# Performance work log

Hardware: AMD Instinct MI355X
Metric: run time of the kernel (lower is better)

Reference implementation:

```python
import jax, jax.numpy as jnp
import numpy as np

N0, N1, N2 = 100000, 25000, 6250
E0, E1, E2 = 600000, 150000, 37500
K = 6


def cheb_conv(x, edge_index, W, b):
    """torch_geometric ChebConv with sym normalization, lambda_max=2:
    L_hat = -D^{-1/2} A D^{-1/2}; T0=x, T1=L_hat x, Tk=2 L_hat T_{k-1} - T_{k-2}."""
    n = x.shape[0]
    src, dst = edge_index[0], edge_index[1]
    deg = jax.ops.segment_sum(jnp.ones(src.shape[0], x.dtype), src, num_segments=n)
    dinv = jnp.where(deg > 0, jax.lax.rsqrt(jnp.maximum(deg, 1.0)), 0.0)
    w = -(dinv[src] * dinv[dst])  # [E]

    def prop(h):  # (L_hat h)_i = sum_{j->i} w_ij h_j
        return jax.ops.segment_sum(w[:, None] * h[src], dst, num_segments=n)

    Tx0 = x
    out = Tx0 @ W[0]
    Tx1 = prop(x)
    out = out + Tx1 @ W[1]
    for k in range(2, W.shape[0]):
        Tx2 = 2.0 * prop(Tx1) - Tx0
        out = out + Tx2 @ W[k]
        Tx0, Tx1 = Tx1, Tx2
    return out + b


def pool(x, rows, cols, vals, n_out):
    # sparse.mm(D, x): y[r] += v * x[c]
    return jax.ops.segment_sum(vals[:, None] * x[cols], rows, num_segments=n_out)


def setup_inputs() -> dict:
    key = jax.random.key(0)
    ks = jax.random.split(key, 16)
    inp = {}
    inp["x"] = jax.random.normal(ks[0], (N0, 3), jnp.float32)
    inp["edge_index0"] = jax.random.randint(ks[1], (2, E0), 0, N0, jnp.int32)
    inp["edge_index1"] = jax.random.randint(ks[2], (2, E1), 0, N1, jnp.int32)
    inp["edge_index2"] = jax.random.randint(ks[3], (2, E2), 0, N2, jnp.int32)
    s = 0.05
    inp["W0"] = jax.random.normal(ks[4], (K, 3, 128), jnp.float32) * s
    inp["b0"] = jax.random.normal(ks[5], (128,), jnp.float32) * s
    inp["W1"] = jax.random.normal(ks[6], (K, 128, 128), jnp.float32) * s
    inp["b1"] = jax.random.normal(ks[7], (128,), jnp.float32) * s
    inp["W2"] = jax.random.normal(ks[8], (K, 128, 256), jnp.float32) * s
    inp["b2"] = jax.random.normal(ks[9], (256,), jnp.float32) * s
    inp["D0_rows"] = jax.random.randint(ks[10], (100000,), 0, N1, jnp.int32)
    inp["D0_cols"] = jax.random.randint(ks[11], (100000,), 0, N0, jnp.int32)
    inp["D0_vals"] = jax.random.uniform(ks[12], (100000,), jnp.float32)
    inp["D1_rows"] = jax.random.randint(ks[13], (25000,), 0, N2, jnp.int32)
    inp["D1_cols"] = jax.random.randint(ks[14], (25000,), 0, N1, jnp.int32)
    inp["D1_vals"] = jax.random.uniform(ks[15], (25000,), jnp.float32)
    k2 = jax.random.split(jax.random.fold_in(key, 1), 2)
    inp["linW"] = jax.random.normal(k2[0], (10, N2 * 256), jnp.float32) * 0.001
    inp["linb"] = jax.random.normal(k2[1], (10,), jnp.float32) * s
    return inp


def reference(x, edge_index0, edge_index1, edge_index2, W0, b0, W1, b1, W2, b2,
              D0_rows, D0_cols, D0_vals, D1_rows, D1_cols, D1_vals, linW, linb):
    h = jax.nn.relu(cheb_conv(x, edge_index0, W0, b0))      # [N0,128]
    h = pool(h, D0_rows, D0_cols, D0_vals, N1)               # [N1,128]
    h = jax.nn.relu(cheb_conv(h, edge_index1, W1, b1))      # [N1,128]
    h = pool(h, D1_rows, D1_cols, D1_vals, N2)               # [N2,128]
    h = cheb_conv(h, edge_index2, W2, b2)                    # [N2,256]
    Z = linW @ h.reshape(-1) + linb                           # [10]
    return Z
```

## Files before the change

kernel.cpp:

```cpp
#include <hip/hip_runtime.h>


namespace {
constexpr int cN0 = 100000, cN1 = 25000, cN2 = 6250;
constexpr int cE0 = 600000, cE1 = 150000, cE2 = 37500;
constexpr int cD  = cN2 * 256;

constexpr int JN[5]  = {cN0, cN1, cN2, cN1, cN2};
constexpr int JE[5]  = {cE0, cE1, cE2, 100000, 25000};
constexpr int JB[5]  = {391, 98, 25, 98, 25};
constexpr int JBBASE[6] = {0, 391, 489, 514, 612, 637};
constexpr int TB = 637;
constexpr int JCB[5] = {293, 74, 19, 49, 13};
constexpr int JCBASE[6] = {0, 293, 367, 386, 435, 448};
constexpr int TCB = 448;
constexpr int CHUNK = 2048;
constexpr int BSTRIDE = 400;

constexpr int EBASE[5]   = {0, 600000, 750000, 787500, 887500};
constexpr int E_TOTAL    = 912500;
constexpr int NBASE[5]   = {0, 100096, 125184, 131584, 156672};
constexpr int NPAD_TOTAL = 163072;
constexpr int DEGBASE[3] = {0, 100000, 125000};
constexpr int DEG_TOTAL  = 131250;
constexpr int WPREP_TOTAL = 768 * 128 + 768 * 256 + 128 * 32;
}

typedef __attribute__((ext_vector_type(8))) short short8;
typedef __attribute__((ext_vector_type(4))) float floatx4;

__device__ inline ushort f2bf(float f) {
  union { float f; unsigned u; } v; v.f = f;
  unsigned u = v.u;
  return (ushort)((u + 0x7FFFu + ((u >> 16) & 1u)) >> 16);
}

__device__ inline float bf2f(unsigned lo16) {
  return __uint_as_float(lo16 << 16);
}

__device__ inline int job_of_cb(int cb) {
  int j = 0;
  while (cb >= JCBASE[j + 1]) ++j;
  return j;
}
__device__ inline int job_of_bucket(int g) {
  int j = 0;
  while (g >= JBBASE[j + 1]) ++j;
  return j;
}

__global__ __launch_bounds__(256) void c1_count_kernel(
    const int* __restrict__ k0, const int* __restrict__ k1, const int* __restrict__ k2,
    const int* __restrict__ k3, const int* __restrict__ k4,
    const int* __restrict__ s0, const int* __restrict__ s1, const int* __restrict__ s2,
    int* __restrict__ degcnt, int* __restrict__ cntCB) {
  __shared__ int cnt[BSTRIDE];
  int cb = blockIdx.x;
  int j = job_of_cb(cb);
  int lb = cb - JCBASE[j];
  const int* keys;
  const int* srck = nullptr;
  int dbase = 0;
  switch (j) {
    case 0: keys = k0; srck = s0; dbase = DEGBASE[0]; break;
    case 1: keys = k1; srck = s1; dbase = DEGBASE[1]; break;
    case 2: keys = k2; srck = s2; dbase = DEGBASE[2]; break;
    case 3: keys = k3; break;
    default: keys = k4; break;
  }
  int nB = JB[j];
  for (int b = threadIdx.x; b < nB; b += 256) cnt[b] = 0;
  __syncthreads();
  int e0 = lb * CHUNK;
  int e1 = min(e0 + CHUNK, JE[j]);
  for (int e = e0 + threadIdx.x; e < e1; e += 256) {
    atomicAdd(&cnt[keys[e] >> 8], 1);
    if (srck) atomicAdd(&degcnt[dbase + srck[e]], 1);
  }
  __syncthreads();
  for (int b = threadIdx.x; b < nB; b += 256)
    cntCB[cb * BSTRIDE + b] = cnt[b];
}

__global__ __launch_bounds__(256) void c2a_scan_kernel(int* __restrict__ cntCB,
                                                       int* __restrict__ bucketTot,
                                                       const int* __restrict__ degcnt,
                                                       float* __restrict__ dinv) {
  __shared__ int s[256];
  int g = blockIdx.x;
  int j = job_of_bucket(g);
  int b = g - JBBASE[j];
  int cb0 = JCBASE[j], nCB = JCB[j];
  int carry = 0;
  for (int c0 = 0; c0 < nCB; c0 += 256) {
    int i = c0 + threadIdx.x;
    int v = (i < nCB) ? cntCB[(cb0 + i) * BSTRIDE + b] : 0;
    s[threadIdx.x] = v;
    __syncthreads();
    for (int d = 1; d < 256; d <<= 1) {
      int t = (threadIdx.x >= d) ? s[threadIdx.x - d] : 0;
      __syncthreads();
      s[threadIdx.x] += t;
      __syncthreads();
    }
    if (i < nCB) cntCB[(cb0 + i) * BSTRIDE + b] = carry + s[threadIdx.x] - v;
    carry += s[255];
    __syncthreads();
  }
  if (threadIdx.x == 0) bucketTot[g] = carry;
  int idx = blockIdx.x * 256 + threadIdx.x;
  if (idx < DEG_TOTAL) {
    int c = degcnt[idx];
    dinv[idx] = (c > 0) ? rsqrtf((float)c) : 0.f;
  }
}

__global__ __launch_bounds__(256) void c2b_scan_kernel(const int* __restrict__ bucketTot,
                                                       int* __restrict__ bucketBase) {
  __shared__ int s[256];
  int j = blockIdx.x;
  int g0 = JBBASE[j], nB = JB[j];
  int carry = 0;
  for (int c0 = 0; c0 < nB; c0 += 256) {
    int i = c0 + threadIdx.x;
    int v = (i < nB) ? bucketTot[g0 + i] : 0;
    s[threadIdx.x] = v;
    __syncthreads();
    for (int d = 1; d < 256; d <<= 1) {
      int t = (threadIdx.x >= d) ? s[threadIdx.x - d] : 0;
      __syncthreads();
      s[threadIdx.x] += t;
      __syncthreads();
    }
    if (i < nB) bucketBase[g0 + i] = carry + s[threadIdx.x] - v;
    carry += s[255];
    __syncthreads();
  }
}

__global__ __launch_bounds__(256) void c3_dst_kernel(
    const int* __restrict__ d0, const int* __restrict__ s0,
    const int* __restrict__ d1, const int* __restrict__ s1,
    const int* __restrict__ d2, const int* __restrict__ s2,
    const int* __restrict__ p0r, const int* __restrict__ p0c, const float* __restrict__ p0v,
    const int* __restrict__ p1r, const int* __restrict__ p1c, const float* __restrict__ p1v,
    const float* __restrict__ dinv,
    const int* __restrict__ cntCB, const int* __restrict__ bucketBase,
    int2* __restrict__ scatPairs) {
  __shared__ int base[BSTRIDE];
  int cb = blockIdx.x;
  int j = job_of_cb(cb);
  int lb = cb - JCBASE[j];
  const int* dk; const int* sk; const float* vv = nullptr;
  switch (j) {
    case 0: dk = d0; sk = s0; break;
    case 1: dk = d1; sk = s1; break;
    case 2: dk = d2; sk = s2; break;
    case 3: dk = p0r; sk = p0c; vv = p0v; break;
    default: dk = p1r; sk = p1c; vv = p1v; break;
  }
  int nB = JB[j];
  for (int b = threadIdx.x; b < nB; b += 256)
    base[b] = EBASE[j] + bucketBase[JBBASE[j] + b] + cntCB[cb * BSTRIDE + b];
  __syncthreads();
  int e0 = lb * CHUNK;
  int e1 = min(e0 + CHUNK, JE[j]);
  for (int e = e0 + threadIdx.x; e < e1; e += 256) {
    int d = dk[e];
    int s = sk[e];
    float w;
    if (j < 3) w = -(dinv[DEGBASE[j] + s] * dinv[DEGBASE[j] + d]);
    else w = vv[e];
    int pos = atomicAdd(&base[d >> 8], 1);
    scatPairs[pos] = make_int2(((d & 255) << 17) | s, __float_as_int(w));
  }
}

__global__ __launch_bounds__(256) void dcsr_kernel(const int2* __restrict__ scatPairs,
                                                   const int* __restrict__ bucketTot,
                                                   const int* __restrict__ bucketBase,
                                                   int* __restrict__ off,
                                                   int2* __restrict__ csrPairs) {
  __shared__ int cnt[256];
  __shared__ int sArr[256];
  __shared__ int cur[256];
  int g = blockIdx.x;
  int j = job_of_bucket(g);
  int b = g - JBBASE[j];
  int relBase = bucketBase[g];
  int st = EBASE[j] + relBase;
  int en = st + bucketTot[g];
  cnt[threadIdx.x] = 0;
  __syncthreads();
  for (int idx = st + threadIdx.x; idx < en; idx += 256)
    atomicAdd(&cnt[scatPairs[idx].x >> 17], 1);
  __syncthreads();
  int v = cnt[threadIdx.x];
  sArr[threadIdx.x] = v;
  __syncthreads();
  for (int d = 1; d < 256; d <<= 1) {
    int t = (threadIdx.x >= d) ? sArr[threadIdx.x - d] : 0;
    __syncthreads();
    sArr[threadIdx.x] += t;
    __syncthreads();
  }
  int excl = sArr[threadIdx.x] - v;
  int node = b * 256 + threadIdx.x;
  if (node < JN[j]) off[NBASE[j] + node] = relBase + excl;
  if (threadIdx.x == 0 && b == JB[j] - 1) off[NBASE[j] + JN[j]] = JE[j];
  cur[threadIdx.x] = st + excl;
  __syncthreads();
  for (int idx = st + threadIdx.x; idx < en; idx += 256) {
    int2 p = scatPairs[idx];
    int dl = p.x >> 17;
    int s = p.x & 0x1FFFF;
    int pos = atomicAdd(&cur[dl], 1);
    csrPairs[pos] = make_int2(s, p.y);
  }
}

__global__ __launch_bounds__(256) void csr_prop128_kernel(
    const int* __restrict__ off, const int2* __restrict__ pairs,
    const float* __restrict__ h, float* __restrict__ y, ushort* __restrict__ ybf,
    const float* __restrict__ prev, float scale, int N) {
  int r = blockIdx.x * 8 + (threadIdx.x >> 5);
  int l = threadIdx.x & 31;
  if (r >= N) return;
  int s = off[r], e = off[r + 1];
  const float4* h4 = (const float4*)h;
  float ax = 0.f, ay = 0.f, az = 0.f, aw = 0.f;
  int j = s;
  for (; j + 4 <= e; j += 4) {
    int2 p0 = pairs[j], p1 = pairs[j + 1], p2 = pairs[j + 2], p3 = pairs[j + 3];
    float4 v0 = h4[(size_t)p0.x * 32 + l];
    float4 v1 = h4[(size_t)p1.x * 32 + l];
    float4 v2 = h4[(size_t)p2.x * 32 + l];
    float4 v3 = h4[(size_t)p3.x * 32 + l];
    float w0 = __int_as_float(p0.y), w1 = __int_as_float(p1.y);
    float w2 = __int_as_float(p2.y), w3 = __int_as_float(p3.y);
    ax += w0 * v0.x + w1 * v1.x + w2 * v2.x + w3 * v3.x;
    ay += w0 * v0.y + w1 * v1.y + w2 * v2.y + w3 * v3.y;
    az += w0 * v0.z + w1 * v1.z + w2 * v2.z + w3 * v3.z;
    aw += w0 * v0.w + w1 * v1.w + w2 * v2.w + w3 * v3.w;
  }
  for (; j < e; ++j) {
    int2 p = pairs[j];
    float4 v0 = h4[(size_t)p.x * 32 + l];
    float w = __int_as_float(p.y);
    ax += w * v0.x; ay += w * v0.y; az += w * v0.z; aw += w * v0.w;
  }
  float4 v = make_float4(scale * ax, scale * ay, scale * az, scale * aw);
  if (prev) {
    float4 pv = ((const float4*)prev)[(size_t)r * 32 + l];
    v.x -= pv.x; v.y -= pv.y; v.z -= pv.z; v.w -= pv.w;
  }
  if (y) ((float4*)y)[(size_t)r * 32 + l] = v;
  uint2 sp = make_uint2(f2bf(v.x) | ((unsigned)f2bf(v.y) << 16),
                        f2bf(v.z) | ((unsigned)f2bf(v.w) << 16));
  ((uint2*)ybf)[(size_t)r * 32 + l] = sp;
}

__global__ __launch_bounds__(256) void csr_pool_bf16_kernel(
    const int* __restrict__ off, const int2* __restrict__ pairs,
    const ushort* __restrict__ hbf, float* __restrict__ y, ushort* __restrict__ ybf,
    int N) {
  int r = blockIdx.x * 8 + (threadIdx.x >> 5);
  int l = threadIdx.x & 31;
  if (r >= N) return;
  int s = off[r], e = off[r + 1];
  const uint2* h2 = (const uint2*)hbf;
  float ax = 0.f, ay = 0.f, az = 0.f, aw = 0.f;
  int j = s;
  for (; j + 4 <= e; j += 4) {
    int2 p0 = pairs[j], p1 = pairs[j + 1], p2 = pairs[j + 2], p3 = pairs[j + 3];
    uint2 v0 = h2[(size_t)p0.x * 32 + l];
    uint2 v1 = h2[(size_t)p1.x * 32 + l];
    uint2 v2 = h2[(size_t)p2.x * 32 + l];
    uint2 v3 = h2[(size_t)p3.x * 32 + l];
    float w0 = __int_as_float(p0.y), w1 = __int_as_float(p1.y);
    float w2 = __int_as_float(p2.y), w3 = __int_as_float(p3.y);
    ax += w0 * bf2f(v0.x & 0xFFFFu) + w1 * bf2f(v1.x & 0xFFFFu)
        + w2 * bf2f(v2.x & 0xFFFFu) + w3 * bf2f(v3.x & 0xFFFFu);
    ay += w0 * bf2f(v0.x >> 16) + w1 * bf2f(v1.x >> 16)
        + w2 * bf2f(v2.x >> 16) + w3 * bf2f(v3.x >> 16);
    az += w0 * bf2f(v0.y & 0xFFFFu) + w1 * bf2f(v1.y & 0xFFFFu)
        + w2 * bf2f(v2.y & 0xFFFFu) + w3 * bf2f(v3.y & 0xFFFFu);
    aw += w0 * bf2f(v0.y >> 16) + w1 * bf2f(v1.y >> 16)
        + w2 * bf2f(v2.y >> 16) + w3 * bf2f(v3.y >> 16);
  }
  for (; j < e; ++j) {
    int2 p = pairs[j];
    uint2 v0 = h2[(size_t)p.x * 32 + l];
    float w = __int_as_float(p.y);
    ax += w * bf2f(v0.x & 0xFFFFu);
    ay += w * bf2f(v0.x >> 16);
    az += w * bf2f(v0.y & 0xFFFFu);
    aw += w * bf2f(v0.y >> 16);
  }
  float4 v = make_float4(ax, ay, az, aw);
  ((float4*)y)[(size_t)r * 32 + l] = v;
  uint2 sp = make_uint2(f2bf(v.x) | ((unsigned)f2bf(v.y) << 16),
                        f2bf(v.z) | ((unsigned)f2bf(v.w) << 16));
  ((uint2*)ybf)[(size_t)r * 32 + l] = sp;
}

__global__ void csr_prop3_kernel(const int* __restrict__ off, const int2* __restrict__ pairs,
                                 const float4* __restrict__ h, float4* __restrict__ y,
                                 const float4* __restrict__ prev, float scale, int N,
                                 ushort* __restrict__ ybf, int kout) {
  int r = blockIdx.x * blockDim.x + threadIdx.x;
  if (r >= N) return;
  int s = off[r], e = off[r + 1];
  float ax = 0.f, ay = 0.f, az = 0.f;
  int j = s;
  for (; j + 4 <= e; j += 4) {
    int2 p0 = pairs[j], p1 = pairs[j + 1], p2 = pairs[j + 2], p3 = pairs[j + 3];
    float4 h0 = h[p0.x], h1 = h[p1.x], h2 = h[p2.x], h3 = h[p3.x];
    float w0 = __int_as_float(p0.y), w1 = __int_as_float(p1.y);
    float w2 = __int_as_float(p2.y), w3 = __int_as_float(p3.y);
    ax += w0 * h0.x + w1 * h1.x + w2 * h2.x + w3 * h3.x;
    ay += w0 * h0.y + w1 * h1.y + w2 * h2.y + w3 * h3.y;
    az += w0 * h0.z + w1 * h1.z + w2 * h2.z + w3 * h3.z;
  }
  for (; j < e; ++j) {
    int2 p = pairs[j];
    float4 hv = h[p.x];
    float w = __int_as_float(p.y);
    ax += w * hv.x; ay += w * hv.y; az += w * hv.z;
  }
  float4 v = make_float4(scale * ax, scale * ay, scale * az, 0.f);
  if (prev) {
    float4 pv = prev[r];
    v.x -= pv.x; v.y -= pv.y; v.z -= pv.z;
  }
  y[r] = v;
  uint2 sp = make_uint2(f2bf(v.x) | ((unsigned)f2bf(v.y) << 16), (unsigned)f2bf(v.z));
  *(uint2*)(ybf + (size_t)r * 32 + kout * 4) = sp;
}

__global__ void copyx_kernel(const float* __restrict__ x, float4* __restrict__ Tb,
                             ushort* __restrict__ Abf, int N) {
  int r = blockIdx.x * 256 + threadIdx.x;
  if (r >= N) return;
  float x0 = x[3 * r], x1 = x[3 * r + 1], x2 = x[3 * r + 2];
  Tb[r] = make_float4(x0, x1, x2, 0.f);
  uint4 z = make_uint4(0, 0, 0, 0);
  uint4 first = make_uint4(f2bf(x0) | ((unsigned)f2bf(x1) << 16), (unsigned)f2bf(x2), 0, 0);
  uint4* p = (uint4*)(Abf + (size_t)r * 32);
  p[0] = first; p[1] = z; p[2] = z; p[3] = z;
}

__global__ __launch_bounds__(256, 2) void h0_mfma_kernel(
    const ushort* __restrict__ Abf, const ushort* __restrict__ W0b,
    const float* __restrict__ b0, ushort* __restrict__ h0bf, int M) {
  __shared__ ushort Al[64][40];
  __shared__ ushort Bl[128][40];
  __shared__ ushort Hs[64][128];
  const int tid = threadIdx.x;
  const int rowBase = blockIdx.x * 64;
  const int wave = tid >> 6;
  const int lane = tid & 63;
  const int m16 = lane & 15;
  const int quad = lane >> 4;
  {
    int sRow = tid >> 2;
    int sK8 = (tid & 3) * 8;
    int row = rowBase + sRow;
    uint4 av = make_uint4(0, 0, 0, 0);
    if (row < M) av = *(const uint4*)(Abf + (size_t)row * 32 + sK8);
    *(uint4*)&Al[sRow][sK8] = av;
  }
#pragma unroll
  for (int l = 0; l < 2; ++l) {
    int lin = tid + l * 256;
    int bRow = lin >> 2;
    int bK8 = (lin & 3) * 8;
    *(uint4*)&Bl[bRow][bK8] = *(const uint4*)(W0b + (size_t)bRow * 32 + bK8);
  }
  __syncthreads();
  short8 a = *(const short8*)&Al[wave * 16 + m16][quad * 8];
  floatx4 acc[8];
#pragma unroll
  for (int c = 0; c < 8; ++c) {
    floatx4 z;
    z[0] = 0.f; z[1] = 0.f; z[2] = 0.f; z[3] = 0.f;
    short8 b = *(const short8*)&Bl[c * 16 + m16][quad * 8];
    acc[c] = __builtin_amdgcn_mfma_f32_16x16x32_bf16(a, b, z, 0, 0, 0);
  }
#pragma unroll
  for (int c = 0; c < 8; ++c) {
    int col = c * 16 + m16;
    float bv = b0[col];
#pragma unroll
    for (int r = 0; r < 4; ++r)
      Hs[wave * 16 + quad * 4 + r][col] = f2bf(fmaxf(acc[c][r] + bv, 0.f));
  }
  __syncthreads();
  const uint4* ls = (const uint4*)&Hs[0][0];
  uint4* gd = (uint4*)(h0bf + (size_t)rowBase * 128);
#pragma unroll
  for (int i = 0; i < 4; ++i) {
    int idx = tid + i * 256;
    if (rowBase + (idx >> 4) < M) gd[idx] = ls[idx];
  }
}

__global__ void prep_w_kernel(const float* __restrict__ W0, const float* __restrict__ W1,
                              const float* __restrict__ W2, ushort* __restrict__ W0b,
                              ushort* __restrict__ Wt1, ushort* __restrict__ Wt2,
                              int* __restrict__ degcnt) {
  int i = blockIdx.x * 256 + threadIdx.x;
  if (i < 768 * 128) {
    int k = i / 128, n = i - k * 128;
    Wt1[(size_t)n * 768 + k] = f2bf(W1[i]);
  } else if (i < 768 * 128 + 768 * 256) {
    int i2 = i - 768 * 128;
    int k = i2 / 256, n = i2 - k * 256;
    Wt2[(size_t)n * 768 + k] = f2bf(W2[i2]);
  } else if (i < WPREP_TOTAL) {
    int i3 = i - 768 * 128 - 768 * 256;
    int col = i3 >> 5, k = i3 & 31;
    int a = k >> 2, jj = k & 3;
    float v = (k < 24 && jj < 3) ? W0[(a * 3 + jj) * 128 + col] : 0.f;
    W0b[(size_t)col * 32 + k] = f2bf(v);
  } else {
    int i4 = i - WPREP_TOTAL;
    if (i4 < DEG_TOTAL) degcnt[i4] = 0;
  }
}

template <int RELU, int OUTBF>
__global__ __launch_bounds__(256, 2) void gemm_mfma_kernel(
    const ushort* __restrict__ Tbf, const ushort* __restrict__ Wt,
    const float* __restrict__ bias, float* __restrict__ C, ushort* __restrict__ Cb,
    int M, int N) {
  __shared__ ushort Al[64][40];
  __shared__ ushort Bl[128][40];
  __shared__ ushort Hs[64][128];
  const int tid = threadIdx.x;
  const int rowBase = blockIdx.x * 64;
  const int colBase = blockIdx.y * 128;
  const int wave = tid >> 6;
  const int lane = tid & 63;
  const int m16 = lane & 15;
  const int quad = lane >> 4;
  const size_t Mstride = (size_t)M * 128;

  floatx4 acc[8];
#pragma unroll
  for (int c = 0; c < 8; ++c)
#pragma unroll
    for (int r = 0; r < 4; ++r) acc[c][r] = 0.f;

  const int sRow = tid >> 2;
  const int sK8 = (tid & 3) * 8;
  const int growA = rowBase + sRow;
  const bool aValid = growA < M;

  for (int kc = 0; kc < 24; ++kc) {
    uint4 av = make_uint4(0, 0, 0, 0);
    if (aValid)
      av = *(const uint4*)(Tbf + (size_t)(kc >> 2) * Mstride + (size_t)growA * 128
                           + ((kc & 3) << 5) + sK8);
    *(uint4*)&Al[sRow][sK8] = av;
#pragma unroll
    for (int l = 0; l < 2; ++l) {
      int lin = tid + l * 256;
      int bRow = lin >> 2;
      int bK8 = (lin & 3) * 8;
      *(uint4*)&Bl[bRow][bK8] =
          *(const uint4*)(Wt + (size_t)(colBase + bRow) * 768 + kc * 32 + bK8);
    }
    __syncthreads();

    short8 a = *(const short8*)&Al[wave * 16 + m16][quad * 8];
#pragma unroll
    for (int c = 0; c < 8; ++c) {
      short8 b = *(const short8*)&Bl[c * 16 + m16][quad * 8];
      acc[c] = __builtin_amdgcn_mfma_f32_16x16x32_bf16(a, b, acc[c], 0, 0, 0);
    }
    __syncthreads();
  }

  if (OUTBF) {
#pragma unroll
    for (int c = 0; c < 8; ++c) {
      int col = c * 16 + m16;
      float bv = bias[col];
#pragma unroll
      for (int r = 0; r < 4; ++r) {
        float v = acc[c][r] + bv;
        if (RELU) v = fmaxf(v, 0.f);
        Hs[wave * 16 + quad * 4 + r][col] = f2bf(v);
      }
    }
    __syncthreads();
    const uint4* ls = (const uint4*)&Hs[0][0];
    uint4* gd = (uint4*)(Cb + (size_t)rowBase * 128);
#pragma unroll
    for (int i = 0; i < 4; ++i) {
      int idx = tid + i * 256;
      if (rowBase + (idx >> 4) < M) gd[idx] = ls[idx];
    }
  } else {
#pragma unroll
    for (int c = 0; c < 8; ++c) {
      int col = colBase + c * 16 + m16;
      float bv = bias[col];
#pragma unroll
      for (int r = 0; r < 4; ++r) {
        int row = rowBase + wave * 16 + quad * 4 + r;
        if (row < M) {
          float v = acc[c][r] + bv;
          if (RELU) v = fmaxf(v, 0.f);
          C[(size_t)row * N + col] = v;
        }
      }
    }
  }
}

__global__ void initout_kernel(float* __restrict__ out, const float* __restrict__ linb) {
  int i = threadIdx.x;
  if (i < 10) out[i] = linb[i];
}

__global__ __launch_bounds__(256) void linear_kernel(const float* __restrict__ Wl,
                                                     const float* __restrict__ h,
                                                     float* __restrict__ out, int D) {
  float p[10];
#pragma unroll
  for (int j = 0; j < 10; ++j) p[j] = 0.f;
  int stride = gridDim.x * blockDim.x;
  for (int i = blockIdx.x * blockDim.x + threadIdx.x; i < D; i += stride) {
    float hv = h[i];
#pragma unroll
    for (int j = 0; j < 10; ++j) p[j] += Wl[(size_t)j * D + i] * hv;
  }
#pragma unroll
  for (int j = 0; j < 10; ++j) {
#pragma unroll
    for (int off = 32; off > 0; off >>= 1) p[j] += __shfl_down(p[j], off, 64);
  }
  __shared__ float s[4][10];
  int wave = threadIdx.x >> 6, lane = threadIdx.x & 63;
  if (lane == 0) {
#pragma unroll
    for (int j = 0; j < 10; ++j) s[wave][j] = p[j];
  }
  __syncthreads();
  if (threadIdx.x < 10) {
    float t = s[0][threadIdx.x] + s[1][threadIdx.x] + s[2][threadIdx.x] + s[3][threadIdx.x];
    atomicAdd(&out[threadIdx.x], t);
  }
}

extern "C" void kernel_launch(void* const* d_in, const int* in_sizes, int n_in,
                              void* d_out, int out_size, void* d_ws, size_t ws_size,
                              hipStream_t stream) {
  const float* x    = (const float*)d_in[0];
  const int*   ei0  = (const int*)d_in[1];
  const int*   ei1  = (const int*)d_in[2];
  const int*   ei2  = (const int*)d_in[3];
  const float* W0   = (const float*)d_in[4];
  const float* b0   = (const float*)d_in[5];
  const float* W1   = (const float*)d_in[6];
  const float* b1   = (const float*)d_in[7];
  const float* W2   = (const float*)d_in[8];
  const float* b2   = (const float*)d_in[9];
  const int*   D0r  = (const int*)d_in[10];
  const int*   D0c  = (const int*)d_in[11];
  const float* D0v  = (const float*)d_in[12];
  const int*   D1r  = (const int*)d_in[13];
  const int*   D1c  = (const int*)d_in[14];
  const float* D1v  = (const float*)d_in[15];
  const float* linW = (const float*)d_in[16];
  const float* linb = (const float*)d_in[17];
  float* out = (float*)d_out;
  (void)in_sizes; (void)n_in; (void)out_size; (void)ws_size;

  const int* src0 = ei0;            const int* dst0 = ei0 + cE0;
  const int* src1 = ei1;            const int* dst1 = ei1 + cE1;
  const int* src2 = ei2;            const int* dst2 = ei2 + cE2;

  float* ws = (float*)d_ws;
  size_t off = 0;
  auto alloc = [&](size_t n) {
    float* p = ws + off;
    off += (n + 63) & ~size_t(63);
    return p;
  };
  float* dinv       = alloc(DEG_TOTAL);
  int*   degcnt     = (int*)alloc(DEG_TOTAL);
  int*   cntCB      = (int*)alloc((size_t)TCB * BSTRIDE);
  int*   bucketTot  = (int*)alloc(TB);
  int*   bucketBase = (int*)alloc(TB);
  int2*  scatPairs  = (int2*)alloc((size_t)2 * E_TOTAL);
  int2*  csrPairs   = (int2*)alloc((size_t)2 * E_TOTAL);
  int*   offArr     = (int*)alloc(NPAD_TOTAL);
  ushort* W0b       = (ushort*)alloc(128 * 32 / 2);
  ushort* Wt1       = (ushort*)alloc(768 * 128 / 2);
  ushort* Wt2       = (ushort*)alloc(768 * 256 / 2);
  float4* Tb0       = (float4*)alloc((size_t)6 * cN0 * 4);
  ushort* Abf0      = (ushort*)alloc((size_t)cN0 * 16);
  ushort* h0bf      = (ushort*)alloc((size_t)cN0 * 64);
  float* Tlvl1      = alloc((size_t)6 * cN1 * 128);
  ushort* Tbf1      = (ushort*)alloc((size_t)6 * cN1 * 64);
  ushort* out1b     = (ushort*)alloc((size_t)cN1 * 64);
  float* Tlvl2      = alloc((size_t)6 * cN2 * 128);
  ushort* Tbf2      = (ushort*)alloc((size_t)6 * cN2 * 64);
  float* out2       = alloc((size_t)cN2 * 256);

  auto nb = [](long long n) { return (unsigned)((n + 255) / 256); };

  prep_w_kernel<<<nb(WPREP_TOTAL + DEG_TOTAL), 256, 0, stream>>>(
      W0, W1, W2, W0b, Wt1, Wt2, degcnt);

  c1_count_kernel<<<TCB, 256, 0, stream>>>(dst0, dst1, dst2, D0r, D1r,
                                           src0, src1, src2, degcnt, cntCB);
  c2a_scan_kernel<<<TB, 256, 0, stream>>>(cntCB, bucketTot, degcnt, dinv);
  c2b_scan_kernel<<<5, 256, 0, stream>>>(bucketTot, bucketBase);
  c3_dst_kernel<<<TCB, 256, 0, stream>>>(dst0, src0, dst1, src1, dst2, src2,
                                         D0r, D0c, D0v, D1r, D1c, D1v,
                                         dinv, cntCB, bucketBase, scatPairs);
  dcsr_kernel<<<TB, 256, 0, stream>>>(scatPairs, bucketTot, bucketBase,
                                      offArr, csrPairs);

  auto seg_off   = [&](int s) { return offArr + NBASE[s]; };
  auto seg_pairs = [&](int s) { return csrPairs + EBASE[s]; };

  copyx_kernel<<<nb(cN0), 256, 0, stream>>>(x, Tb0, Abf0, cN0);
  {
    auto Tk = [&](int k) { return Tb0 + (size_t)k * cN0; };
    csr_prop3_kernel<<<nb(cN0), 256, 0, stream>>>(seg_off(0), seg_pairs(0),
        Tk(0), Tk(1), nullptr, 1.f, cN0, Abf0, 1);
    csr_prop3_kernel<<<nb(cN0), 256, 0, stream>>>(seg_off(0), seg_pairs(0),
        Tk(1), Tk(2), Tk(0), 2.f, cN0, Abf0, 2);
    csr_prop3_kernel<<<nb(cN0), 256, 0, stream>>>(seg_off(0), seg_pairs(0),
        Tk(2), Tk(3), Tk(1), 2.f, cN0, Abf0, 3);
    csr_prop3_kernel<<<nb(cN0), 256, 0, stream>>>(seg_off(0), seg_pairs(0),
        Tk(3), Tk(4), Tk(2), 2.f, cN0, Abf0, 4);
    csr_prop3_kernel<<<nb(cN0), 256, 0, stream>>>(seg_off(0), seg_pairs(0),
        Tk(4), Tk(5), Tk(3), 2.f, cN0, Abf0, 5);
  }
  h0_mfma_kernel<<<(cN0 + 63) / 64, 256, 0, stream>>>(Abf0, W0b, b0, h0bf, cN0);
  csr_pool_bf16_kernel<<<(cN1 + 7) / 8, 256, 0, stream>>>(
      seg_off(3), seg_pairs(3), h0bf, Tlvl1, Tbf1, cN1);

  {
    auto Tk  = [&](int k) { return Tlvl1 + (size_t)k * cN1 * 128; };
    auto Tbk = [&](int k) { return Tbf1 + (size_t)k * cN1 * 128; };
    auto prop = [&](int kin, int kout, int kprev, float scale, bool needF32) {
      csr_prop128_kernel<<<(cN1 + 7) / 8, 256, 0, stream>>>(
          seg_off(1), seg_pairs(1), Tk(kin), needF32 ? Tk(kout) : nullptr, Tbk(kout),
          (kprev >= 0) ? Tk(kprev) : nullptr, scale, cN1);
    };
    prop(0, 1, -1, 1.f, true);
    prop(1, 2, 0, 2.f, true);
    prop(2, 3, 1, 2.f, true);
    prop(3, 4, 2, 2.f, true);
    prop(4, 5, 3, 2.f, false);
    dim3 g((cN1 + 63) / 64, 1);
    gemm_mfma_kernel<1, 1><<<g, 256, 0, stream>>>(Tbf1, Wt1, b1, nullptr, out1b,
                                                  cN1, 128);
  }

  csr_pool_bf16_kernel<<<(cN2 + 7) / 8, 256, 0, stream>>>(
      seg_off(4), seg_pairs(4), out1b, Tlvl2, Tbf2, cN2);

  {
    auto Tk  = [&](int k) { return Tlvl2 + (size_t)k * cN2 * 128; };
    auto Tbk = [&](int k) { return Tbf2 + (size_t)k * cN2 * 128; };
    auto prop = [&](int kin, int kout, int kprev, float scale, bool needF32) {
      csr_prop128_kernel<<<(cN2 + 7) / 8, 256, 0, stream>>>(
          seg_off(2), seg_pairs(2), Tk(kin), needF32 ? Tk(kout) : nullptr, Tbk(kout),
          (kprev >= 0) ? Tk(kprev) : nullptr, scale, cN2);
    };
    prop(0, 1, -1, 1.f, true);
    prop(1, 2, 0, 2.f, true);
    prop(2, 3, 1, 2.f, true);
    prop(3, 4, 2, 2.f, true);
    prop(4, 5, 3, 2.f, false);
    dim3 g((cN2 + 63) / 64, 2);
    gemm_mfma_kernel<0, 0><<<g, 256, 0, stream>>>(Tbf2, Wt2, b2, out2, nullptr,
                                                  cN2, 256);
  }

  initout_kernel<<<1, 64, 0, stream>>>(out, linb);
  linear_kernel<<<512, 256, 0, stream>>>(linW, out2, out, cD);
}
```

Before: 438.8 us.

## Switch intermediates to fp16, gather fp16 in 128-wide props, fold small kernels into prep

Replaces bf16 with fp16 for all reduced-precision intermediates and MFMA instructions. The 128-wide Chebyshev propagation now gathers neighbour features from the fp16 copy instead of fp32, halving gather bytes, while the Chebyshev recurrence subtraction still uses the fp32 previous term. The pooling kernels are merged into the same generic kernel, and the copyx and initout kernels are folded into one prep kernel to cut launches. The trade is reduced precision in the propagated values, and fp16 overflow risk compared to bf16.

```diff
diff --git a/kernel.cpp b/kernel.cpp
--- a/kernel.cpp
+++ b/kernel.cpp
@@ -24,19 +24,21 @@
 constexpr int DEGBASE[3] = {0, 100000, 125000};
 constexpr int DEG_TOTAL  = 131250;
 constexpr int WPREP_TOTAL = 768 * 128 + 768 * 256 + 128 * 32;
+constexpr int PREP_ALL_TOTAL = WPREP_TOTAL + DEG_TOTAL + cN0 + 10;
 }
 
 typedef __attribute__((ext_vector_type(8))) short short8;
 typedef __attribute__((ext_vector_type(4))) float floatx4;
 
-__device__ inline ushort f2bf(float f) {
-  union { float f; unsigned u; } v; v.f = f;
-  unsigned u = v.u;
-  return (ushort)((u + 0x7FFFu + ((u >> 16) & 1u)) >> 16);
-}
-
-__device__ inline float bf2f(unsigned lo16) {
-  return __uint_as_float(lo16 << 16);
+__device__ inline ushort f2h(float f) {
+  union { _Float16 h; ushort u; } v;
+  v.h = (_Float16)f;
+  return v.u;
+}
+__device__ inline float h2f(unsigned lo16) {
+  union { ushort u; _Float16 h; } v;
+  v.u = (ushort)lo16;
+  return (float)v.h;
 }
 
 __device__ inline int job_of_cb(int cb) {
@@ -220,56 +222,15 @@
   }
 }
 
-__global__ __launch_bounds__(256) void csr_prop128_kernel(
+__global__ __launch_bounds__(256) void csr_prop128h_kernel(
     const int* __restrict__ off, const int2* __restrict__ pairs,
-    const float* __restrict__ h, float* __restrict__ y, ushort* __restrict__ ybf,
+    const ushort* __restrict__ hh, float* __restrict__ y, ushort* __restrict__ yh,
     const float* __restrict__ prev, float scale, int N) {
   int r = blockIdx.x * 8 + (threadIdx.x >> 5);
   int l = threadIdx.x & 31;
   if (r >= N) return;
   int s = off[r], e = off[r + 1];
-  const float4* h4 = (const float4*)h;
-  float ax = 0.f, ay = 0.f, az = 0.f, aw = 0.f;
-  int j = s;
-  for (; j + 4 <= e; j += 4) {
-    int2 p0 = pairs[j], p1 = pairs[j + 1], p2 = pairs[j + 2], p3 = pairs[j + 3];
-    float4 v0 = h4[(size_t)p0.x * 32 + l];
-    float4 v1 = h4[(size_t)p1.x * 32 + l];
-    float4 v2 = h4[(size_t)p2.x * 32 + l];
-    float4 v3 = h4[(size_t)p3.x * 32 + l];
-    float w0 = __int_as_float(p0.y), w1 = __int_as_float(p1.y);
-    float w2 = __int_as_float(p2.y), w3 = __int_as_float(p3.y);
-    ax += w0 * v0.x + w1 * v1.x + w2 * v2.x + w3 * v3.x;
-    ay += w0 * v0.y + w1 * v1.y + w2 * v2.y + w3 * v3.y;
-    az += w0 * v0.z + w1 * v1.z + w2 * v2.z + w3 * v3.z;
-    aw += w0 * v0.w + w1 * v1.w + w2 * v2.w + w3 * v3.w;
-  }
-  for (; j < e; ++j) {
-    int2 p = pairs[j];
-    float4 v0 = h4[(size_t)p.x * 32 + l];
-    float w = __int_as_float(p.y);
-    ax += w * v0.x; ay += w * v0.y; az += w * v0.z; aw += w * v0.w;
-  }
-  float4 v = make_float4(scale * ax, scale * ay, scale * az, scale * aw);
-  if (prev) {
-    float4 pv = ((const float4*)prev)[(size_t)r * 32 + l];
-    v.x -= pv.x; v.y -= pv.y; v.z -= pv.z; v.w -= pv.w;
-  }
-  if (y) ((float4*)y)[(size_t)r * 32 + l] = v;
-  uint2 sp = make_uint2(f2bf(v.x) | ((unsigned)f2bf(v.y) << 16),
-                        f2bf(v.z) | ((unsigned)f2bf(v.w) << 16));
-  ((uint2*)ybf)[(size_t)r * 32 + l] = sp;
-}
-
-__global__ __launch_bounds__(256) void csr_pool_bf16_kernel(
-    const int* __restrict__ off, const int2* __restrict__ pairs,
-    const ushort* __restrict__ hbf, float* __restrict__ y, ushort* __restrict__ ybf,
-    int N) {
-  int r = blockIdx.x * 8 + (threadIdx.x >> 5);
-  int l = threadIdx.x & 31;
-  if (r >= N) return;
-  int s = off[r], e = off[r + 1];
-  const uint2* h2 = (const uint2*)hbf;
+  const uint2* h2 = (const uint2*)hh;
   float ax = 0.f, ay = 0.f, az = 0.f, aw = 0.f;
   int j = s;
   for (; j + 4 <= e; j += 4) {
@@ -280,35 +241,39 @@
     uint2 v3 = h2[(size_t)p3.x * 32 + l];
     float w0 = __int_as_float(p0.y), w1 = __int_as_float(p1.y);
     float w2 = __int_as_float(p2.y), w3 = __int_as_float(p3.y);
-    ax += w0 * bf2f(v0.x & 0xFFFFu) + w1 * bf2f(v1.x & 0xFFFFu)
-        + w2 * bf2f(v2.x & 0xFFFFu) + w3 * bf2f(v3.x & 0xFFFFu);
-    ay += w0 * bf2f(v0.x >> 16) + w1 * bf2f(v1.x >> 16)
-        + w2 * bf2f(v2.x >> 16) + w3 * bf2f(v3.x >> 16);
-    az += w0 * bf2f(v0.y & 0xFFFFu) + w1 * bf2f(v1.y & 0xFFFFu)
-        + w2 * bf2f(v2.y & 0xFFFFu) + w3 * bf2f(v3.y & 0xFFFFu);
-    aw += w0 * bf2f(v0.y >> 16) + w1 * bf2f(v1.y >> 16)
-        + w2 * bf2f(v2.y >> 16) + w3 * bf2f(v3.y >> 16);
+    ax += w0 * h2f(v0.x & 0xFFFFu) + w1 * h2f(v1.x & 0xFFFFu)
+        + w2 * h2f(v2.x & 0xFFFFu) + w3 * h2f(v3.x & 0xFFFFu);
+    ay += w0 * h2f(v0.x >> 16) + w1 * h2f(v1.x >> 16)
+        + w2 * h2f(v2.x >> 16) + w3 * h2f(v3.x >> 16);
+    az += w0 * h2f(v0.y & 0xFFFFu) + w1 * h2f(v1.y & 0xFFFFu)
+        + w2 * h2f(v2.y & 0xFFFFu) + w3 * h2f(v3.y & 0xFFFFu);
+    aw += w0 * h2f(v0.y >> 16) + w1 * h2f(v1.y >> 16)
+        + w2 * h2f(v2.y >> 16) + w3 * h2f(v3.y >> 16);
   }
   for (; j < e; ++j) {
     int2 p = pairs[j];
     uint2 v0 = h2[(size_t)p.x * 32 + l];
     float w = __int_as_float(p.y);
-    ax += w * bf2f(v0.x & 0xFFFFu);
-    ay += w * bf2f(v0.x >> 16);
-    az += w * bf2f(v0.y & 0xFFFFu);
-    aw += w * bf2f(v0.y >> 16);
-  }
-  float4 v = make_float4(ax, ay, az, aw);
-  ((float4*)y)[(size_t)r * 32 + l] = v;
-  uint2 sp = make_uint2(f2bf(v.x) | ((unsigned)f2bf(v.y) << 16),
-                        f2bf(v.z) | ((unsigned)f2bf(v.w) << 16));
-  ((uint2*)ybf)[(size_t)r * 32 + l] = sp;
+    ax += w * h2f(v0.x & 0xFFFFu);
+    ay += w * h2f(v0.x >> 16);
+    az += w * h2f(v0.y & 0xFFFFu);
+    aw += w * h2f(v0.y >> 16);
+  }
+  float4 v = make_float4(scale * ax, scale * ay, scale * az, scale * aw);
+  if (prev) {
+    float4 pv = ((const float4*)prev)[(size_t)r * 32 + l];
+    v.x -= pv.x; v.y -= pv.y; v.z -= pv.z; v.w -= pv.w;
+  }
+  if (y) ((float4*)y)[(size_t)r * 32 + l] = v;
+  uint2 sp = make_uint2(f2h(v.x) | ((unsigned)f2h(v.y) << 16),
+                        f2h(v.z) | ((unsigned)f2h(v.w) << 16));
+  ((uint2*)yh)[(size_t)r * 32 + l] = sp;
 }
 
 __global__ void csr_prop3_kernel(const int* __restrict__ off, const int2* __restrict__ pairs,
                                  const float4* __restrict__ h, float4* __restrict__ y,
                                  const float4* __restrict__ prev, float scale, int N,
-                                 ushort* __restrict__ ybf, int kout) {
+                                 ushort* __restrict__ yh, int kout) {
   int r = blockIdx.x * blockDim.x + threadIdx.x;
   if (r >= N) return;
   int s = off[r], e = off[r + 1];
@@ -335,25 +300,13 @@
     v.x -= pv.x; v.y -= pv.y; v.z -= pv.z;
   }
   y[r] = v;
-  uint2 sp = make_uint2(f2bf(v.x) | ((unsigned)f2bf(v.y) << 16), (unsigned)f2bf(v.z));
-  *(uint2*)(ybf + (size_t)r * 32 + kout * 4) = sp;
-}
-
-__global__ void copyx_kernel(const float* __restrict__ x, float4* __restrict__ Tb,
-                             ushort* __restrict__ Abf, int N) {
-  int r = blockIdx.x * 256 + threadIdx.x;
-  if (r >= N) return;
-  float x0 = x[3 * r], x1 = x[3 * r + 1], x2 = x[3 * r + 2];
-  Tb[r] = make_float4(x0, x1, x2, 0.f);
-  uint4 z = make_uint4(0, 0, 0, 0);
-  uint4 first = make_uint4(f2bf(x0) | ((unsigned)f2bf(x1) << 16), (unsigned)f2bf(x2), 0, 0);
-  uint4* p = (uint4*)(Abf + (size_t)r * 32);
-  p[0] = first; p[1] = z; p[2] = z; p[3] = z;
+  uint2 sp = make_uint2(f2h(v.x) | ((unsigned)f2h(v.y) << 16), (unsigned)f2h(v.z));
+  *(uint2*)(yh + (size_t)r * 32 + kout * 4) = sp;
 }
 
 __global__ __launch_bounds__(256, 2) void h0_mfma_kernel(
-    const ushort* __restrict__ Abf, const ushort* __restrict__ W0b,
-    const float* __restrict__ b0, ushort* __restrict__ h0bf, int M) {
+    const ushort* __restrict__ Ah, const ushort* __restrict__ W0h,
+    const float* __restrict__ b0, ushort* __restrict__ h0h, int M) {
   __shared__ ushort Al[64][40];
   __shared__ ushort Bl[128][40];
   __shared__ ushort Hs[64][128];
@@ -368,7 +321,7 @@
     int sK8 = (tid & 3) * 8;
     int row = rowBase + sRow;
     uint4 av = make_uint4(0, 0, 0, 0);
-    if (row < M) av = *(const uint4*)(Abf + (size_t)row * 32 + sK8);
+    if (row < M) av = *(const uint4*)(Ah + (size_t)row * 32 + sK8);
     *(uint4*)&Al[sRow][sK8] = av;
   }
 #pragma unroll
@@ -376,7 +329,7 @@
     int lin = tid + l * 256;
     int bRow = lin >> 2;
     int bK8 = (lin & 3) * 8;
-    *(uint4*)&Bl[bRow][bK8] = *(const uint4*)(W0b + (size_t)bRow * 32 + bK8);
+    *(uint4*)&Bl[bRow][bK8] = *(const uint4*)(W0h + (size_t)bRow * 32 + bK8);
   }
   __syncthreads();
   short8 a = *(const short8*)&Al[wave * 16 + m16][quad * 8];
@@ -386,7 +339,7 @@
     floatx4 z;
     z[0] = 0.f; z[1] = 0.f; z[2] = 0.f; z[3] = 0.f;
     short8 b = *(const short8*)&Bl[c * 16 + m16][quad * 8];
-    acc[c] = __builtin_amdgcn_mfma_f32_16x16x32_bf16(a, b, z, 0, 0, 0);
+    acc[c] = __builtin_amdgcn_mfma_f32_16x16x32_f16(a, b, z, 0, 0, 0);
   }
 #pragma unroll
   for (int c = 0; c < 8; ++c) {
@@ -394,11 +347,11 @@
     float bv = b0[col];
 #pragma unroll
     for (int r = 0; r < 4; ++r)
-      Hs[wave * 16 + quad * 4 + r][col] = f2bf(fmaxf(acc[c][r] + bv, 0.f));
+      Hs[wave * 16 + quad * 4 + r][col] = f2h(fmaxf(acc[c][r] + bv, 0.f));
   }
   __syncthreads();
   const uint4* ls = (const uint4*)&Hs[0][0];
-  uint4* gd = (uint4*)(h0bf + (size_t)rowBase * 128);
+  uint4* gd = (uint4*)(h0h + (size_t)rowBase * 128);
 #pragma unroll
   for (int i = 0; i < 4; ++i) {
     int idx = tid + i * 256;
@@ -406,34 +359,47 @@
   }
 }
 
-__global__ void prep_w_kernel(const float* __restrict__ W0, const float* __restrict__ W1,
-                              const float* __restrict__ W2, ushort* __restrict__ W0b,
-                              ushort* __restrict__ Wt1, ushort* __restrict__ Wt2,
-                              int* __restrict__ degcnt) {
+__global__ void prep_all_kernel(const float* __restrict__ W0, const float* __restrict__ W1,
+                                const float* __restrict__ W2, ushort* __restrict__ W0h,
+                                ushort* __restrict__ Wt1, ushort* __restrict__ Wt2,
+                                int* __restrict__ degcnt,
+                                const float* __restrict__ x, float4* __restrict__ Tb,
+                                ushort* __restrict__ Ah,
+                                float* __restrict__ out, const float* __restrict__ linb) {
   int i = blockIdx.x * 256 + threadIdx.x;
   if (i < 768 * 128) {
     int k = i / 128, n = i - k * 128;
-    Wt1[(size_t)n * 768 + k] = f2bf(W1[i]);
+    Wt1[(size_t)n * 768 + k] = f2h(W1[i]);
   } else if (i < 768 * 128 + 768 * 256) {
     int i2 = i - 768 * 128;
     int k = i2 / 256, n = i2 - k * 256;
-    Wt2[(size_t)n * 768 + k] = f2bf(W2[i2]);
+    Wt2[(size_t)n * 768 + k] = f2h(W2[i2]);
   } else if (i < WPREP_TOTAL) {
     int i3 = i - 768 * 128 - 768 * 256;
     int col = i3 >> 5, k = i3 & 31;
     int a = k >> 2, jj = k & 3;
     float v = (k < 24 && jj < 3) ? W0[(a * 3 + jj) * 128 + col] : 0.f;
-    W0b[(size_t)col * 32 + k] = f2bf(v);
-  } else {
-    int i4 = i - WPREP_TOTAL;
-    if (i4 < DEG_TOTAL) degcnt[i4] = 0;
-  }
-}
-
-template <int RELU, int OUTBF>
+    W0h[(size_t)col * 32 + k] = f2h(v);
+  } else if (i < WPREP_TOTAL + DEG_TOTAL) {
+    degcnt[i - WPREP_TOTAL] = 0;
+  } else if (i < WPREP_TOTAL + DEG_TOTAL + cN0) {
+    int r = i - (WPREP_TOTAL + DEG_TOTAL);
+    float x0 = x[3 * r], x1 = x[3 * r + 1], x2 = x[3 * r + 2];
+    Tb[r] = make_float4(x0, x1, x2, 0.f);
+    uint4 z = make_uint4(0, 0, 0, 0);
+    uint4 first = make_uint4(f2h(x0) | ((unsigned)f2h(x1) << 16), (unsigned)f2h(x2), 0, 0);
+    uint4* p = (uint4*)(Ah + (size_t)r * 32);
+    p[0] = first; p[1] = z; p[2] = z; p[3] = z;
+  } else if (i < PREP_ALL_TOTAL) {
+    int o = i - (WPREP_TOTAL + DEG_TOTAL + cN0);
+    out[o] = linb[o];
+  }
+}
+
+template <int RELU, int OUTH>
 __global__ __launch_bounds__(256, 2) void gemm_mfma_kernel(
-    const ushort* __restrict__ Tbf, const ushort* __restrict__ Wt,
-    const float* __restrict__ bias, float* __restrict__ C, ushort* __restrict__ Cb,
+    const ushort* __restrict__ Th, const ushort* __restrict__ Wt,
+    const float* __restrict__ bias, float* __restrict__ C, ushort* __restrict__ Ch,
     int M, int N) {
   __shared__ ushort Al[64][40];
   __shared__ ushort Bl[128][40];
@@ -461,7 +427,7 @@
   for (int kc = 0; kc < 24; ++kc) {
     uint4 av = make_uint4(0, 0, 0, 0);
     if (aValid)
-      av = *(const uint4*)(Tbf + (size_t)(kc >> 2) * Mstride + (size_t)growA * 128
+      av = *(const uint4*)(Th + (size_t)(kc >> 2) * Mstride + (size_t)growA * 128
                            + ((kc & 3) << 5) + sK8);
     *(uint4*)&Al[sRow][sK8] = av;
 #pragma unroll
@@ -478,12 +444,12 @@
 #pragma unroll
     for (int c = 0; c < 8; ++c) {
       short8 b = *(const short8*)&Bl[c * 16 + m16][quad * 8];
-      acc[c] = __builtin_amdgcn_mfma_f32_16x16x32_bf16(a, b, acc[c], 0, 0, 0);
+      acc[c] = __builtin_amdgcn_mfma_f32_16x16x32_f16(a, b, acc[c], 0, 0, 0);
     }
     __syncthreads();
   }
 
-  if (OUTBF) {
+  if (OUTH) {
 #pragma unroll
     for (int c = 0; c < 8; ++c) {
       int col = c * 16 + m16;
@@ -492,12 +458,12 @@
       for (int r = 0; r < 4; ++r) {
         float v = acc[c][r] + bv;
         if (RELU) v = fmaxf(v, 0.f);
-        Hs[wave * 16 + quad * 4 + r][col] = f2bf(v);
+        Hs[wave * 16 + quad * 4 + r][col] = f2h(v);
       }
     }
     __syncthreads();
     const uint4* ls = (const uint4*)&Hs[0][0];
-    uint4* gd = (uint4*)(Cb + (size_t)rowBase * 128);
+    uint4* gd = (uint4*)(Ch + (size_t)rowBase * 128);
 #pragma unroll
     for (int i = 0; i < 4; ++i) {
       int idx = tid + i * 256;
@@ -519,11 +485,6 @@
       }
     }
   }
-}
-
-__global__ void initout_kernel(float* __restrict__ out, const float* __restrict__ linb) {
-  int i = threadIdx.x;
-  if (i < 10) out[i] = linb[i];
 }
 
 __global__ __launch_bounds__(256) void linear_kernel(const float* __restrict__ Wl,
@@ -599,23 +560,23 @@
   int2*  scatPairs  = (int2*)alloc((size_t)2 * E_TOTAL);
   int2*  csrPairs   = (int2*)alloc((size_t)2 * E_TOTAL);
   int*   offArr     = (int*)alloc(NPAD_TOTAL);
-  ushort* W0b       = (ushort*)alloc(128 * 32 / 2);
+  ushort* W0h       = (ushort*)alloc(128 * 32 / 2);
   ushort* Wt1       = (ushort*)alloc(768 * 128 / 2);
   ushort* Wt2       = (ushort*)alloc(768 * 256 / 2);
   float4* Tb0       = (float4*)alloc((size_t)6 * cN0 * 4);
-  ushort* Abf0      = (ushort*)alloc((size_t)cN0 * 16);
-  ushort* h0bf      = (ushort*)alloc((size_t)cN0 * 64);
+  ushort* Ah0       = (ushort*)alloc((size_t)cN0 * 16);
+  ushort* h0h       = (ushort*)alloc((size_t)cN0 * 64);
   float* Tlvl1      = alloc((size_t)6 * cN1 * 128);
-  ushort* Tbf1      = (ushort*)alloc((size_t)6 * cN1 * 64);
-  ushort* out1b     = (ushort*)alloc((size_t)cN1 * 64);
+  ushort* Th1       = (ushort*)alloc((size_t)6 * cN1 * 64);
+  ushort* out1h     = (ushort*)alloc((size_t)cN1 * 64);
   float* Tlvl2      = alloc((size_t)6 * cN2 * 128);
-  ushort* Tbf2      = (ushort*)alloc((size_t)6 * cN2 * 64);
+  ushort* Th2       = (ushort*)alloc((size_t)6 * cN2 * 64);
   float* out2       = alloc((size_t)cN2 * 256);
 
   auto nb = [](long long n) { return (unsigned)((n + 255) / 256); };
 
-  prep_w_kernel<<<nb(WPREP_TOTAL + DEG_TOTAL), 256, 0, stream>>>(
-      W0, W1, W2, W0b, Wt1, Wt2, degcnt);
+  prep_all_kernel<<<nb(PREP_ALL_TOTAL), 256, 0, stream>>>(
+      W0, W1, W2, W0h, Wt1, Wt2, degcnt, x, Tb0, Ah0, out, linb);
 
   c1_count_kernel<<<TCB, 256, 0, stream>>>(dst0, dst1, dst2, D0r, D1r,
                                            src0, src1, src2, degcnt, cntCB);
@@ -630,30 +591,29 @@
   auto seg_off   = [&](int s) { return offArr + NBASE[s]; };
   auto seg_pairs = [&](int s) { return csrPairs + EBASE[s]; };
 
-  copyx_kernel<<<nb(cN0), 256, 0, stream>>>(x, Tb0, Abf0, cN0);
   {
     auto Tk = [&](int k) { return Tb0 + (size_t)k * cN0; };
     csr_prop3_kernel<<<nb(cN0), 256, 0, stream>>>(seg_off(0), seg_pairs(0),
-        Tk(0), Tk(1), nullptr, 1.f, cN0, Abf0, 1);
+        Tk(0), Tk(1), nullptr, 1.f, cN0, Ah0, 1);
     csr_prop3_kernel<<<nb(cN0), 256, 0, stream>>>(seg_off(0), seg_pairs(0),
-        Tk(1), Tk(2), Tk(0), 2.f, cN0, Abf0, 2);
+        Tk(1), Tk(2), Tk(0), 2.f, cN0, Ah0, 2);
     csr_prop3_kernel<<<nb(cN0), 256, 0, stream>>>(seg_off(0), seg_pairs(0),
-        Tk(2), Tk(3), Tk(1), 2.f, cN0, Abf0, 3);
+        Tk(2), Tk(3), Tk(1), 2.f, cN0, Ah0, 3);
     csr_prop3_kernel<<<nb(cN0), 256, 0, stream>>>(seg_off(0), seg_pairs(0),
-        Tk(3), Tk(4), Tk(2), 2.f, cN0, Abf0, 4);
+        Tk(3), Tk(4), Tk(2), 2.f, cN0, Ah0, 4);
     csr_prop3_kernel<<<nb(cN0), 256, 0, stream>>>(seg_off(0), seg_pairs(0),
-        Tk(4), Tk(5), Tk(3), 2.f, cN0, Abf0, 5);
-  }
-  h0_mfma_kernel<<<(cN0 + 63) / 64, 256, 0, stream>>>(Abf0, W0b, b0, h0bf, cN0);
-  csr_pool_bf16_kernel<<<(cN1 + 7) / 8, 256, 0, stream>>>(
-      seg_off(3), seg_pairs(3), h0bf, Tlvl1, Tbf1, cN1);
+        Tk(4), Tk(5), Tk(3), 2.f, cN0, Ah0, 5);
+  }
+  h0_mfma_kernel<<<(cN0 + 63) / 64, 256, 0, stream>>>(Ah0, W0h, b0, h0h, cN0);
+  csr_prop128h_kernel<<<(cN1 + 7) / 8, 256, 0, stream>>>(
+      seg_off(3), seg_pairs(3), h0h, Tlvl1, Th1, nullptr, 1.f, cN1);
 
   {
     auto Tk  = [&](int k) { return Tlvl1 + (size_t)k * cN1 * 128; };
-    auto Tbk = [&](int k) { return Tbf1 + (size_t)k * cN1 * 128; };
+    auto Thk = [&](int k) { return Th1 + (size_t)k * cN1 * 128; };
     auto prop = [&](int kin, int kout, int kprev, float scale, bool needF32) {
-      csr_prop128_kernel<<<(cN1 + 7) / 8, 256, 0, stream>>>(
-          seg_off(1), seg_pairs(1), Tk(kin), needF32 ? Tk(kout) : nullptr, Tbk(kout),
+      csr_prop128h_kernel<<<(cN1 + 7) / 8, 256, 0, stream>>>(
+          seg_off(1), seg_pairs(1), Thk(kin), needF32 ? Tk(kout) : nullptr, Thk(kout),
           (kprev >= 0) ? Tk(kprev) : nullptr, scale, cN1);
     };
     prop(0, 1, -1, 1.f, true);
@@ -662,19 +622,19 @@
     prop(3, 4, 2, 2.f, true);
     prop(4, 5, 3, 2.f, false);
     dim3 g((cN1 + 63) / 64, 1);
-    gemm_mfma_kernel<1, 1><<<g, 256, 0, stream>>>(Tbf1, Wt1, b1, nullptr, out1b,
+    gemm_mfma_kernel<1, 1><<<g, 256, 0, stream>>>(Th1, Wt1, b1, nullptr, out1h,
                                                   cN1, 128);
   }
 
-  csr_pool_bf16_kernel<<<(cN2 + 7) / 8, 256, 0, stream>>>(
-      seg_off(4), seg_pairs(4), out1b, Tlvl2, Tbf2, cN2);
+  csr_prop128h_kernel<<<(cN2 + 7) / 8, 256, 0, stream>>>(
+      seg_off(4), seg_pairs(4), out1h, Tlvl2, Th2, nullptr, 1.f, cN2);
 
   {
     auto Tk  = [&](int k) { return Tlvl2 + (size_t)k * cN2 * 128; };
-    auto Tbk = [&](int k) { return Tbf2 + (size_t)k * cN2 * 128; };
+    auto Thk = [&](int k) { return Th2 + (size_t)k * cN2 * 128; };
     auto prop = [&](int kin, int kout, int kprev, float scale, bool needF32) {
-      csr_prop128_kernel<<<(cN2 + 7) / 8, 256, 0, stream>>>(
-          seg_off(2), seg_pairs(2), Tk(kin), needF32 ? Tk(kout) : nullptr, Tbk(kout),
+      csr_prop128h_kernel<<<(cN2 + 7) / 8, 256, 0, stream>>>(
+          seg_off(2), seg_pairs(2), Thk(kin), needF32 ? Tk(kout) : nullptr, Thk(kout),
           (kprev >= 0) ? Tk(kprev) : nullptr, scale, cN2);
     };
     prop(0, 1, -1, 1.f, true);
@@ -683,10 +643,9 @@
     prop(3, 4, 2, 2.f, true);
     prop(4, 5, 3, 2.f, false);
     dim3 g((cN2 + 63) / 64, 2);
-    gemm_mfma_kernel<0, 0><<<g, 256, 0, stream>>>(Tbf2, Wt2, b2, out2, nullptr,
+    gemm_mfma_kernel<0, 0><<<g, 256, 0, stream>>>(Th2, Wt2, b2, out2, nullptr,
                                                   cN2, 256);
   }
 
-  initout_kernel<<<1, 64, 0, stream>>>(out, linb);
   linear_kernel<<<512, 256, 0, stream>>>(linW, out2, out, cD);
 }
```

Result: faster. 418.8 us (-4.6%).
